# Performance work log

Hardware: AMD Instinct MI355X
Metric: run time of the kernel (lower is better)

## Reference

```python
import jax, jax.numpy as jnp
import numpy as np

B, L, D, H1, OUT, MAX_W = 16, 128, 768, 770, 40, 30


def _span_mask():
    # valid spans: i <= j and width < MAX_W (structured sparsity over the L x L grid)
    ii, jj = np.meshgrid(np.arange(L), np.arange(L), indexing='ij')
    return ((jj >= ii) & (jj - ii < MAX_W)).astype(np.int32)


def setup_inputs():
    key = jax.random.key(0)
    ks = jax.random.split(key, 5)
    hidden_states = jax.random.normal(ks[0], (B, L + 1, D), dtype=jnp.float32)
    rng = np.random.default_rng(0)
    starts = rng.integers(0, L - MAX_W, size=(B,))
    ends = starts + rng.integers(0, MAX_W, size=(B,))
    pred_spans = jnp.asarray(np.stack([starts, ends], axis=1), dtype=jnp.int32)
    span_mask = jnp.asarray(_span_mask())
    W1 = 0.02 * jax.random.normal(ks[1], (2 * D + 1, H1), dtype=jnp.float32)
    b1 = jax.random.normal(ks[2], (H1,), dtype=jnp.float32)
    W2 = 0.02 * jax.random.normal(ks[3], (H1, OUT), dtype=jnp.float32)
    b2 = jax.random.normal(ks[4], (OUT,), dtype=jnp.float32)
    return dict(hidden_states=hidden_states, pred_spans=pred_spans, token_num=L,
                span_available_indication_matrix=span_mask,
                W1=W1, b1=b1, W2=W2, b2=b2)


def reference(hidden_states, pred_spans, token_num, span_available_indication_matrix, W1, b1, W2, b2):
    # span mask is an integer constant -> resolve valid (i, j) pairs on host
    mask = np.asarray(span_available_indication_matrix)
    vi, vj = np.nonzero(mask == 1)            # [n_valid] each
    vi_j = jnp.asarray(vi)
    vj_j = jnp.asarray(vj)
    vecs = hidden_states[:, 1:token_num + 1, :]  # token t -> hidden[:, t+1, :], [B, L, D]
    xi = vecs[:, vi_j, :]                        # [B, n_valid, D] gather of span-start vecs
    xj = vecs[:, vj_j, :]                        # [B, n_valid, D] gather of span-end vecs
    # pred_indications: 2 if span == pred span; 1 if strictly inside it (i<=j); else 0
    s = pred_spans[:, 0:1]
    e = pred_spans[:, 1:2]
    i_ = vi_j[None, :]
    j_ = vj_j[None, :]
    exact = (i_ == s) & (j_ == e)
    inside = (i_ >= s) & (j_ <= e) & (i_ <= j_)
    ind = jnp.where(exact, 2.0, jnp.where(inside, 1.0, 0.0)).astype(hidden_states.dtype)  # [B, n_valid]
    # Linear over concat([xi, xj, ind]) expressed as split matmuls (avoids materializing concat)
    W1i, W1j, w1c = W1[:D], W1[D:2 * D], W1[2 * D]
    h = (jnp.einsum('bnd,dh->bnh', xi, W1i)
         + jnp.einsum('bnd,dh->bnh', xj, W1j)
         + ind[..., None] * w1c + b1)
    h = jax.nn.relu(h)
    logits = jnp.einsum('bnh,ho->bno', h, W2) + b2   # [B, n_valid, OUT]
    return jax.nn.log_softmax(logits, axis=-1)
```

## Files before the change

### kernel.cpp

```cpp
#include <hip/hip_runtime.h>
#include <math.h>

#define B_ 16
#define L_ 128
#define D_ 768
#define H1_ 770
#define OUT_ 40
#define NPAIRS 3405
#define NLOG 1540
#define YSB 1552
#define VOFFB 776
#define KPAD 800
#define NPAD 48
#define W1TROWS 1600
#define NTILES 252
#define NKS 25

typedef __attribute__((ext_vector_type(8))) short bf16x8;
typedef __attribute__((ext_vector_type(8))) unsigned short u16x8;
typedef __attribute__((ext_vector_type(4))) float f32x4;
typedef __attribute__((ext_vector_type(4))) unsigned int u32x4;

__device__ inline unsigned short f2bf(float f) {
  unsigned int u = __builtin_bit_cast(unsigned int, f);
  u += 0x7fffu + ((u >> 16) & 1u);
  return (unsigned short)(u >> 16);
}
__device__ inline float bf2f(unsigned short x) {
  return __builtin_bit_cast(float, (unsigned int)x << 16);
}

#if __has_builtin(__builtin_amdgcn_cvt_pk_bf16_f32)
typedef __attribute__((ext_vector_type(2))) __bf16 bf16x2_t;
__device__ inline unsigned int pack_bf16(float lo, float hi) {
  bf16x2_t r = __builtin_amdgcn_cvt_pk_bf16_f32(lo, hi);
  return __builtin_bit_cast(unsigned int, r);
}
#else
__device__ inline unsigned int pack_bf16(float lo, float hi) {
  return (unsigned int)f2bf(lo) | ((unsigned int)f2bf(hi) << 16);
}
#endif

typedef const __attribute__((address_space(1))) void* gas_t;
typedef __attribute__((address_space(3))) void* las_t;
__device__ inline void gl2lds16(const void* g, void* l) {
  __builtin_amdgcn_global_load_lds((gas_t)g, (las_t)l, 16, 0, 0);
}

#define NB_X 1536
#define NB_W 160
#define NB_T 1200

__global__ __launch_bounds__(256) void prep_all(
    const float* __restrict__ hidden, const float* __restrict__ W1,
    const float* __restrict__ b1, const float* __restrict__ W2,
    unsigned short* __restrict__ Xb, unsigned short* __restrict__ W1T,
    unsigned short* __restrict__ Bswz, float* __restrict__ Cv)
{
  __shared__ float t[32][33];
  int bx = blockIdx.x;
  const int tid = threadIdx.x;

  if (bx < NB_X) {
    int idx = bx * 256 + tid;
    int m = idx / 192;
    int c = idx - m * 192;
    float4 f = *(const float4*)(hidden + (size_t)(m + (m >> 7) + 1) * D_ + c * 4);
    ushort4 o;
    o.x = f2bf(f.x); o.y = f2bf(f.y); o.z = f2bf(f.z); o.w = f2bf(f.w);
    *(ushort4*)(Xb + (size_t)m * D_ + c * 4) = o;
    return;
  }
  bx -= NB_X;
  if (bx < NB_W) {
    int idx = bx * 256 + tid;
    if (idx < NKS * 3 * 512) {
      int ks = idx / 1536;
      int rem = idx - ks * 1536;
      int f = rem / 512;
      int l = (rem - f * 512) >> 3;
      int e = rem & 7;
      int n = f * 16 + (l & 15);
      int k = ks * 32 + (l >> 4) * 8 + e;
      float v = (n < OUT_ && k < H1_) ? W2[k * OUT_ + n] : 0.f;
      Bswz[idx] = f2bf(v);
    } else if (idx < NKS * 3 * 512 + 3 * KPAD) {
      int c = idx - NKS * 3 * 512;
      int tt = c / KPAD, k = c - tt * KPAD;
      const float* w1c = W1 + 1536 * H1_;
      Cv[c] = (k < H1_) ? (b1[k] + (float)tt * w1c[k]) : 0.f;
    }
    return;
  }
  bx -= NB_W;
  const int tx = tid & 31, ty = tid >> 5;
  const int n0 = (bx % 50) * 32, k0 = (bx / 50) * 32;
  #pragma unroll
  for (int r = 0; r < 4; ++r) {
    int k = k0 + ty + r * 8, n = n0 + tx;
    float v = 0.f;
    if (n < H1_)       v = W1[k * H1_ + n];
    else if (n < NLOG) v = W1[(D_ + k) * H1_ + (n - H1_)];
    t[ty + r * 8][tx] = v;
  }
  __syncthreads();
  #pragma unroll
  for (int r = 0; r < 4; ++r) {
    int n = n0 + ty + r * 8, k = k0 + tx;
    W1T[(size_t)n * D_ + k] = f2bf(t[tx][ty + r * 8]);
  }
}

__global__ __launch_bounds__(256) void gemm1_mfma(
    const unsigned short* __restrict__ Xb, const unsigned short* __restrict__ W1T,
    unsigned short* __restrict__ Yb)
{
  __shared__ unsigned short As[2][64][64];
  __shared__ unsigned short Bs[2][64][64];
  const int tid = threadIdx.x;
  const int lane = tid & 63, w = tid >> 6;
  const int lm = lane & 15, q = lane >> 4;
  const int row0 = blockIdx.y * 64, col0 = blockIdx.x * 64;
  const int m0 = (w >> 1) * 32, n0 = (w & 1) * 32;

  const int srow = w * 16 + (lane >> 3);
  const int schunk = (lane & 7) * 8;
  const unsigned short* ga = Xb  + (size_t)(row0 + srow) * D_ + schunk;
  const unsigned short* gb = W1T + (size_t)(col0 + srow) * D_ + schunk;

  f32x4 acc[2][2] = {};

  auto stage = [&](int k0, int b) {
    gl2lds16(ga + k0,          &As[b][w * 16][0]);
    gl2lds16(ga + k0 + 8 * D_, &As[b][w * 16 + 8][0]);
    gl2lds16(gb + k0,          &Bs[b][w * 16][0]);
    gl2lds16(gb + k0 + 8 * D_, &Bs[b][w * 16 + 8][0]);
  };

  stage(0, 0);
  for (int it = 0; it < 12; ++it) {
    const int cur = it & 1;
    __syncthreads();
    if (it < 11) stage((it + 1) * 64, cur ^ 1);
    #pragma unroll
    for (int ks = 0; ks < 2; ++ks) {
      bf16x8 a0 = *(const bf16x8*)&As[cur][m0 + lm]     [ks * 32 + q * 8];
      bf16x8 a1 = *(const bf16x8*)&As[cur][m0 + 16 + lm][ks * 32 + q * 8];
      bf16x8 b0 = *(const bf16x8*)&Bs[cur][n0 + lm]     [ks * 32 + q * 8];
      bf16x8 b1 = *(const bf16x8*)&Bs[cur][n0 + 16 + lm][ks * 32 + q * 8];
      acc[0][0] = __builtin_amdgcn_mfma_f32_16x16x32_bf16(a0, b0, acc[0][0], 0, 0, 0);
      acc[0][1] = __builtin_amdgcn_mfma_f32_16x16x32_bf16(a0, b1, acc[0][1], 0, 0, 0);
      acc[1][0] = __builtin_amdgcn_mfma_f32_16x16x32_bf16(a1, b0, acc[1][0], 0, 0, 0);
      acc[1][1] = __builtin_amdgcn_mfma_f32_16x16x32_bf16(a1, b1, acc[1][1], 0, 0, 0);
    }
  }

  #pragma unroll
  for (int ti = 0; ti < 2; ++ti) {
    #pragma unroll
    for (int tj = 0; tj < 2; ++tj) {
      int col = col0 + n0 + tj * 16 + lm;
      if (col >= NLOG) continue;
      int pc = (col < H1_) ? col : col + (VOFFB - H1_);
      #pragma unroll
      for (int r = 0; r < 4; ++r) {
        int row = row0 + m0 + ti * 16 + q * 4 + r;
        Yb[(size_t)row * YSB + pc] = f2bf(acc[ti][tj][r]);
      }
    }
  }
}

__device__ inline void tile_decode(int T, int& ti, int& d) {
  if (T < 216) { ti = T / 9; d = T - ti * 9; }
  else {
    int m = T - 216; int r = 24, w = 8;
    while (m >= w) { m -= w; --w; ++r; }
    ti = r; d = m;
  }
}
__device__ inline int pair_rank(int i, int j) {
  return (i < 99) ? i * 30 + (j - i)
                  : NPAIRS - (128 - i) * (129 - i) / 2 + (j - i);
}

__global__ __launch_bounds__(256) void pair_mfma(
    const unsigned short* __restrict__ Yb, const int* __restrict__ spans,
    const unsigned short* __restrict__ Bswz, const float* __restrict__ Cv,
    const float* __restrict__ b2, float* __restrict__ out)
{
  const int tid = threadIdx.x;
  const int bb = blockIdx.y;
  const int lane = tid & 63, w = tid >> 6;
  const int lm = lane & 15, q = lane >> 4;

  int ti, d;
  tile_decode(blockIdx.x * 4 + w, ti, d);
  const int i0 = ti * 4, j0 = (ti + d) * 4;

  const int ai = i0 + (lm & 3);
  const int aj = j0 + (lm >> 2);
  const int s = spans[2 * bb], e = spans[2 * bb + 1];
  const int ind = (ai == s && aj == e) ? 2 : ((ai >= s && aj <= e) ? 1 : 0);

  const unsigned short* uptr = Yb + (size_t)(bb * L_ + ai) * YSB + q * 8;
  const unsigned short* vptr = Yb + (size_t)(bb * L_ + aj) * YSB + VOFFB + q * 8;
  const float* cptr = Cv + ind * KPAD + q * 8;
  const unsigned short* bbase = Bswz + lane * 8;

  f32x4 acc0 = {}, acc1 = {}, acc2 = {};

  #pragma unroll 5
  for (int ks = 0; ks < NKS; ++ks) {
    const int ko = ks * 32;
    u16x8 uu = *(const u16x8*)(uptr + ko);
    u16x8 vv = *(const u16x8*)(vptr + ko);
    float4 c0 = *(const float4*)(cptr + ko);
    float4 c1 = *(const float4*)(cptr + ko + 4);
    float h0 = fmaxf(bf2f(uu[0]) + bf2f(vv[0]) + c0.x, 0.f);
    float h1 = fmaxf(bf2f(uu[1]) + bf2f(vv[1]) + c0.y, 0.f);
    float h2 = fmaxf(bf2f(uu[2]) + bf2f(vv[2]) + c0.z, 0.f);
    float h3 = fmaxf(bf2f(uu[3]) + bf2f(vv[3]) + c0.w, 0.f);
    float h4 = fmaxf(bf2f(uu[4]) + bf2f(vv[4]) + c1.x, 0.f);
    float h5 = fmaxf(bf2f(uu[5]) + bf2f(vv[5]) + c1.y, 0.f);
    float h6 = fmaxf(bf2f(uu[6]) + bf2f(vv[6]) + c1.z, 0.f);
    float h7 = fmaxf(bf2f(uu[7]) + bf2f(vv[7]) + c1.w, 0.f);
    u32x4 hp;
    hp[0] = pack_bf16(h0, h1);
    hp[1] = pack_bf16(h2, h3);
    hp[2] = pack_bf16(h4, h5);
    hp[3] = pack_bf16(h6, h7);
    bf16x8 a = __builtin_bit_cast(bf16x8, hp);
    bf16x8 bf0 = *(const bf16x8*)(bbase + (size_t)(ks * 3 + 0) * 512);
    bf16x8 bf1 = *(const bf16x8*)(bbase + (size_t)(ks * 3 + 1) * 512);
    bf16x8 bf2v = *(const bf16x8*)(bbase + (size_t)(ks * 3 + 2) * 512);
    acc0 = __builtin_amdgcn_mfma_f32_16x16x32_bf16(a, bf0, acc0, 0, 0, 0);
    acc1 = __builtin_amdgcn_mfma_f32_16x16x32_bf16(a, bf1, acc1, 0, 0, 0);
    acc2 = __builtin_amdgcn_mfma_f32_16x16x32_bf16(a, bf2v, acc2, 0, 0, 0);
  }

  const float b2v0 = b2[lm];
  const float b2v1 = b2[16 + lm];
  const float b2v2 = (lm < 8) ? b2[32 + lm] : 0.f;
  const int oi = i0 , oj = j0 + q;

  #pragma unroll
  for (int r = 0; r < 4; ++r) {
    float l0 = acc0[r] + b2v0;
    float l1 = acc1[r] + b2v1;
    float l2 = (lm < 8) ? (acc2[r] + b2v2) : -INFINITY;
    float mx = fmaxf(fmaxf(l0, l1), l2);
    mx = fmaxf(mx, __shfl_xor(mx, 1));
    mx = fmaxf(mx, __shfl_xor(mx, 2));
    mx = fmaxf(mx, __shfl_xor(mx, 4));
    mx = fmaxf(mx, __shfl_xor(mx, 8));
    float sm = expf(l0 - mx) + expf(l1 - mx) + ((lm < 8) ? expf(l2 - mx) : 0.f);
    sm += __shfl_xor(sm, 1);
    sm += __shfl_xor(sm, 2);
    sm += __shfl_xor(sm, 4);
    sm += __shfl_xor(sm, 8);
    float lsd = mx + logf(sm);

    int pi_ = oi + r, pj_ = oj;
    if (pj_ >= pi_ && (pj_ - pi_) < 30) {
      float* op = out + ((size_t)bb * NPAIRS + pair_rank(pi_, pj_)) * OUT_;
      op[lm]      = l0 - lsd;
      op[16 + lm] = l1 - lsd;
      if (lm < 8) op[32 + lm] = l2 - lsd;
    }
  }
}

extern "C" void kernel_launch(void* const* d_in, const int* in_sizes, int n_in,
                              void* d_out, int out_size, void* d_ws, size_t ws_size,
                              hipStream_t stream) {
  const float* hidden = (const float*)d_in[0];
  const int*   spans  = (const int*)d_in[1];
  const float* W1 = (const float*)d_in[4];
  const float* b1 = (const float*)d_in[5];
  const float* W2 = (const float*)d_in[6];
  const float* b2 = (const float*)d_in[7];
  float* out = (float*)d_out;

  char* base = (char*)d_ws;
  size_t off = 0;
  auto take = [&](size_t bytes) {
    char* p = base + off;
    off = (off + bytes + 255) & ~(size_t)255;
    return p;
  };
  unsigned short* Yb   = (unsigned short*)take((size_t)2049 * YSB * 2);
  unsigned short* Xb   = (unsigned short*)take((size_t)2048 * D_ * 2);
  unsigned short* W1T  = (unsigned short*)take((size_t)W1TROWS * D_ * 2);
  unsigned short* Bswz = (unsigned short*)take((size_t)NKS * 3 * 512 * 2);
  float*          Cv   = (float*)take((size_t)3 * KPAD * 4);

  prep_all<<<dim3(NB_X + NB_W + NB_T), 256, 0, stream>>>(
      hidden, W1, b1, W2, Xb, W1T, Bswz, Cv);
  gemm1_mfma<<<dim3(25, 32), 256, 0, stream>>>(Xb, W1T, Yb);
  pair_mfma<<<dim3(63, B_), 256, 0, stream>>>(Yb, spans, Bswz, Cv, b2, out);
}
```

Baseline: 135.1 us.

## Fuse three kernels into one cooperative persistent kernel with grid syncs

```diff
diff --git a/kernel.cpp b/kernel.cpp
--- a/kernel.cpp
+++ b/kernel.cpp
@@ -1,5 +1,8 @@
 #include <hip/hip_runtime.h>
+#include <hip/hip_cooperative_groups.h>
 #include <math.h>
+
+namespace cg = cooperative_groups;
 
 #define B_ 16
 #define L_ 128
@@ -11,10 +14,16 @@
 #define YSB 1552
 #define VOFFB 776
 #define KPAD 800
-#define NPAD 48
 #define W1TROWS 1600
-#define NTILES 252
 #define NKS 25
+#define NCU_ 256
+
+#define NB_X 1536
+#define NB_W 160
+#define NB_T 1200
+#define NB_A (NB_X + NB_W + NB_T)
+#define NB_B 800
+#define NB_C 1008
 
 typedef __attribute__((ext_vector_type(8))) short bf16x8;
 typedef __attribute__((ext_vector_type(8))) unsigned short u16x8;
@@ -48,33 +57,36 @@
   __builtin_amdgcn_global_load_lds((gas_t)g, (las_t)l, 16, 0, 0);
 }
 
-#define NB_X 1536
-#define NB_W 160
-#define NB_T 1200
-
-__global__ __launch_bounds__(256) void prep_all(
-    const float* __restrict__ hidden, const float* __restrict__ W1,
-    const float* __restrict__ b1, const float* __restrict__ W2,
-    unsigned short* __restrict__ Xb, unsigned short* __restrict__ W1T,
-    unsigned short* __restrict__ Bswz, float* __restrict__ Cv)
-{
-  __shared__ float t[32][33];
-  int bx = blockIdx.x;
-  const int tid = threadIdx.x;
-
-  if (bx < NB_X) {
-    int idx = bx * 256 + tid;
+__device__ inline void tile_decode(int T, int& ti, int& d) {
+  if (T < 216) { ti = T / 9; d = T - ti * 9; }
+  else {
+    int m = T - 216; int r = 24, w = 8;
+    while (m >= w) { m -= w; --w; ++r; }
+    ti = r; d = m;
+  }
+}
+__device__ inline int pair_rank(int i, int j) {
+  return (i < 99) ? i * 30 + (j - i)
+                  : NPAIRS - (128 - i) * (129 - i) / 2 + (j - i);
+}
+
+__device__ inline void phaseA_unit(
+    int u, int tid, const float* __restrict__ hidden,
+    const float* __restrict__ W1, const float* __restrict__ b1,
+    const float* __restrict__ W2, unsigned short* __restrict__ Xb,
+    unsigned short* __restrict__ W1T, unsigned short* __restrict__ Bswz,
+    float* __restrict__ Cv, float (*t)[33])
+{
+  if (u < NB_X) {
+    int idx = u * 256 + tid;
     int m = idx / 192;
     int c = idx - m * 192;
     float4 f = *(const float4*)(hidden + (size_t)(m + (m >> 7) + 1) * D_ + c * 4);
     ushort4 o;
     o.x = f2bf(f.x); o.y = f2bf(f.y); o.z = f2bf(f.z); o.w = f2bf(f.w);
     *(ushort4*)(Xb + (size_t)m * D_ + c * 4) = o;
-    return;
-  }
-  bx -= NB_X;
-  if (bx < NB_W) {
-    int idx = bx * 256 + tid;
+  } else if (u < NB_X + NB_W) {
+    int idx = (u - NB_X) * 256 + tid;
     if (idx < NKS * 3 * 512) {
       int ks = idx / 1536;
       int rem = idx - ks * 1536;
@@ -91,39 +103,37 @@
       const float* w1c = W1 + 1536 * H1_;
       Cv[c] = (k < H1_) ? (b1[k] + (float)tt * w1c[k]) : 0.f;
     }
-    return;
-  }
-  bx -= NB_W;
-  const int tx = tid & 31, ty = tid >> 5;
-  const int n0 = (bx % 50) * 32, k0 = (bx / 50) * 32;
-  #pragma unroll
-  for (int r = 0; r < 4; ++r) {
-    int k = k0 + ty + r * 8, n = n0 + tx;
-    float v = 0.f;
-    if (n < H1_)       v = W1[k * H1_ + n];
-    else if (n < NLOG) v = W1[(D_ + k) * H1_ + (n - H1_)];
-    t[ty + r * 8][tx] = v;
-  }
-  __syncthreads();
-  #pragma unroll
-  for (int r = 0; r < 4; ++r) {
-    int n = n0 + ty + r * 8, k = k0 + tx;
-    W1T[(size_t)n * D_ + k] = f2bf(t[tx][ty + r * 8]);
-  }
-}
-
-__global__ __launch_bounds__(256) void gemm1_mfma(
-    const unsigned short* __restrict__ Xb, const unsigned short* __restrict__ W1T,
-    unsigned short* __restrict__ Yb)
-{
-  __shared__ unsigned short As[2][64][64];
-  __shared__ unsigned short Bs[2][64][64];
-  const int tid = threadIdx.x;
+  } else {
+    int bx = u - NB_X - NB_W;
+    const int tx = tid & 31, ty = tid >> 5;
+    const int n0 = (bx % 50) * 32, k0 = (bx / 50) * 32;
+    #pragma unroll
+    for (int r = 0; r < 4; ++r) {
+      int k = k0 + ty + r * 8, n = n0 + tx;
+      float v = 0.f;
+      if (n < H1_)       v = W1[k * H1_ + n];
+      else if (n < NLOG) v = W1[(D_ + k) * H1_ + (n - H1_)];
+      t[ty + r * 8][tx] = v;
+    }
+    __syncthreads();
+    #pragma unroll
+    for (int r = 0; r < 4; ++r) {
+      int n = n0 + ty + r * 8, k = k0 + tx;
+      W1T[(size_t)n * D_ + k] = f2bf(t[tx][ty + r * 8]);
+    }
+    __syncthreads();
+  }
+}
+
+__device__ inline void phaseB_unit(
+    int u, int tid, const unsigned short* __restrict__ Xb,
+    const unsigned short* __restrict__ W1T, unsigned short* __restrict__ Yb,
+    unsigned short (*As)[64], unsigned short (*Bs)[64])
+{
   const int lane = tid & 63, w = tid >> 6;
   const int lm = lane & 15, q = lane >> 4;
-  const int row0 = blockIdx.y * 64, col0 = blockIdx.x * 64;
+  const int row0 = (u / 25) * 64, col0 = (u % 25) * 64;
   const int m0 = (w >> 1) * 32, n0 = (w & 1) * 32;
-
   const int srow = w * 16 + (lane >> 3);
   const int schunk = (lane & 7) * 8;
   const unsigned short* ga = Xb  + (size_t)(row0 + srow) * D_ + schunk;
@@ -131,29 +141,24 @@
 
   f32x4 acc[2][2] = {};
 
-  auto stage = [&](int k0, int b) {
-    gl2lds16(ga + k0,          &As[b][w * 16][0]);
-    gl2lds16(ga + k0 + 8 * D_, &As[b][w * 16 + 8][0]);
-    gl2lds16(gb + k0,          &Bs[b][w * 16][0]);
-    gl2lds16(gb + k0 + 8 * D_, &Bs[b][w * 16 + 8][0]);
-  };
-
-  stage(0, 0);
-  for (int it = 0; it < 12; ++it) {
-    const int cur = it & 1;
+  for (int k0 = 0; k0 < D_; k0 += 64) {
+    gl2lds16(ga + k0,          &As[w * 16][0]);
+    gl2lds16(ga + k0 + 8 * D_, &As[w * 16 + 8][0]);
+    gl2lds16(gb + k0,          &Bs[w * 16][0]);
+    gl2lds16(gb + k0 + 8 * D_, &Bs[w * 16 + 8][0]);
     __syncthreads();
-    if (it < 11) stage((it + 1) * 64, cur ^ 1);
     #pragma unroll
     for (int ks = 0; ks < 2; ++ks) {
-      bf16x8 a0 = *(const bf16x8*)&As[cur][m0 + lm]     [ks * 32 + q * 8];
-      bf16x8 a1 = *(const bf16x8*)&As[cur][m0 + 16 + lm][ks * 32 + q * 8];
-      bf16x8 b0 = *(const bf16x8*)&Bs[cur][n0 + lm]     [ks * 32 + q * 8];
-      bf16x8 b1 = *(const bf16x8*)&Bs[cur][n0 + 16 + lm][ks * 32 + q * 8];
+      bf16x8 a0 = *(const bf16x8*)&As[m0 + lm]     [ks * 32 + q * 8];
+      bf16x8 a1 = *(const bf16x8*)&As[m0 + 16 + lm][ks * 32 + q * 8];
+      bf16x8 b0 = *(const bf16x8*)&Bs[n0 + lm]     [ks * 32 + q * 8];
+      bf16x8 b1 = *(const bf16x8*)&Bs[n0 + 16 + lm][ks * 32 + q * 8];
       acc[0][0] = __builtin_amdgcn_mfma_f32_16x16x32_bf16(a0, b0, acc[0][0], 0, 0, 0);
       acc[0][1] = __builtin_amdgcn_mfma_f32_16x16x32_bf16(a0, b1, acc[0][1], 0, 0, 0);
       acc[1][0] = __builtin_amdgcn_mfma_f32_16x16x32_bf16(a1, b0, acc[1][0], 0, 0, 0);
       acc[1][1] = __builtin_amdgcn_mfma_f32_16x16x32_bf16(a1, b1, acc[1][1], 0, 0, 0);
     }
+    __syncthreads();
   }
 
   #pragma unroll
@@ -172,31 +177,17 @@
   }
 }
 
-__device__ inline void tile_decode(int T, int& ti, int& d) {
-  if (T < 216) { ti = T / 9; d = T - ti * 9; }
-  else {
-    int m = T - 216; int r = 24, w = 8;
-    while (m >= w) { m -= w; --w; ++r; }
-    ti = r; d = m;
-  }
-}
-__device__ inline int pair_rank(int i, int j) {
-  return (i < 99) ? i * 30 + (j - i)
-                  : NPAIRS - (128 - i) * (129 - i) / 2 + (j - i);
-}
-
-__global__ __launch_bounds__(256) void pair_mfma(
-    const unsigned short* __restrict__ Yb, const int* __restrict__ spans,
-    const unsigned short* __restrict__ Bswz, const float* __restrict__ Cv,
-    const float* __restrict__ b2, float* __restrict__ out)
-{
-  const int tid = threadIdx.x;
-  const int bb = blockIdx.y;
+__device__ inline void phaseC_unit(
+    int u, int tid, const unsigned short* __restrict__ Yb,
+    const int* __restrict__ spans, const unsigned short* __restrict__ Bswz,
+    const float* __restrict__ Cv, const float* __restrict__ b2,
+    float* __restrict__ out)
+{
   const int lane = tid & 63, w = tid >> 6;
   const int lm = lane & 15, q = lane >> 4;
-
+  const int bb = u / 63;
   int ti, d;
-  tile_decode(blockIdx.x * 4 + w, ti, d);
+  tile_decode((u % 63) * 4 + w, ti, d);
   const int i0 = ti * 4, j0 = (ti + d) * 4;
 
   const int ai = i0 + (lm & 3);
@@ -211,21 +202,25 @@
 
   f32x4 acc0 = {}, acc1 = {}, acc2 = {};
 
+  u16x8 uu = *(const u16x8*)(uptr);
+  u16x8 vv = *(const u16x8*)(vptr);
+
   #pragma unroll 5
   for (int ks = 0; ks < NKS; ++ks) {
     const int ko = ks * 32;
-    u16x8 uu = *(const u16x8*)(uptr + ko);
-    u16x8 vv = *(const u16x8*)(vptr + ko);
+    u16x8 cu = uu, cw = vv;
+    uu = *(const u16x8*)(uptr + ko + 32);
+    vv = *(const u16x8*)(vptr + ko + 32);
     float4 c0 = *(const float4*)(cptr + ko);
     float4 c1 = *(const float4*)(cptr + ko + 4);
-    float h0 = fmaxf(bf2f(uu[0]) + bf2f(vv[0]) + c0.x, 0.f);
-    float h1 = fmaxf(bf2f(uu[1]) + bf2f(vv[1]) + c0.y, 0.f);
-    float h2 = fmaxf(bf2f(uu[2]) + bf2f(vv[2]) + c0.z, 0.f);
-    float h3 = fmaxf(bf2f(uu[3]) + bf2f(vv[3]) + c0.w, 0.f);
-    float h4 = fmaxf(bf2f(uu[4]) + bf2f(vv[4]) + c1.x, 0.f);
-    float h5 = fmaxf(bf2f(uu[5]) + bf2f(vv[5]) + c1.y, 0.f);
-    float h6 = fmaxf(bf2f(uu[6]) + bf2f(vv[6]) + c1.z, 0.f);
-    float h7 = fmaxf(bf2f(uu[7]) + bf2f(vv[7]) + c1.w, 0.f);
+    float h0 = fmaxf(bf2f(cu[0]) + bf2f(cw[0]) + c0.x, 0.f);
+    float h1 = fmaxf(bf2f(cu[1]) + bf2f(cw[1]) + c0.y, 0.f);
+    float h2 = fmaxf(bf2f(cu[2]) + bf2f(cw[2]) + c0.z, 0.f);
+    float h3 = fmaxf(bf2f(cu[3]) + bf2f(cw[3]) + c0.w, 0.f);
+    float h4 = fmaxf(bf2f(cu[4]) + bf2f(cw[4]) + c1.x, 0.f);
+    float h5 = fmaxf(bf2f(cu[5]) + bf2f(cw[5]) + c1.y, 0.f);
+    float h6 = fmaxf(bf2f(cu[6]) + bf2f(cw[6]) + c1.z, 0.f);
+    float h7 = fmaxf(bf2f(cu[7]) + bf2f(cw[7]) + c1.w, 0.f);
     u32x4 hp;
     hp[0] = pack_bf16(h0, h1);
     hp[1] = pack_bf16(h2, h3);
@@ -243,7 +238,6 @@
   const float b2v0 = b2[lm];
   const float b2v1 = b2[16 + lm];
   const float b2v2 = (lm < 8) ? b2[32 + lm] : 0.f;
-  const int oi = i0 , oj = j0 + q;
 
   #pragma unroll
   for (int r = 0; r < 4; ++r) {
@@ -262,7 +256,7 @@
     sm += __shfl_xor(sm, 8);
     float lsd = mx + logf(sm);
 
-    int pi_ = oi + r, pj_ = oj;
+    int pi_ = i0 + r, pj_ = j0 + q;
     if (pj_ >= pi_ && (pj_ - pi_) < 30) {
       float* op = out + ((size_t)bb * NPAIRS + pair_rank(pi_, pj_)) * OUT_;
       op[lm]      = l0 - lsd;
@@ -270,6 +264,69 @@
       if (lm < 8) op[32 + lm] = l2 - lsd;
     }
   }
+}
+
+__global__ __launch_bounds__(256, 2) void fused_all(
+    const float* __restrict__ hidden, const int* __restrict__ spans,
+    const float* __restrict__ W1, const float* __restrict__ b1,
+    const float* __restrict__ W2, const float* __restrict__ b2,
+    float* __restrict__ out,
+    unsigned short* __restrict__ Xb, unsigned short* __restrict__ W1T,
+    unsigned short* __restrict__ Bswz, float* __restrict__ Cv,
+    unsigned short* __restrict__ Yb)
+{
+  __shared__ union __align__(16) SM {
+    float t[32][33];
+    unsigned short ab[2][64][64];
+  } sm;
+  cg::grid_group grid = cg::this_grid();
+  const int tid = threadIdx.x;
+  const int G = gridDim.x;
+
+  for (int u = blockIdx.x; u < NB_A; u += G)
+    phaseA_unit(u, tid, hidden, W1, b1, W2, Xb, W1T, Bswz, Cv, sm.t);
+
+  __builtin_amdgcn_fence(__ATOMIC_SEQ_CST, "agent");
+  grid.sync();
+  __builtin_amdgcn_fence(__ATOMIC_SEQ_CST, "agent");
+  __syncthreads();
+
+  for (int u = blockIdx.x; u < NB_B; u += G)
+    phaseB_unit(u, tid, Xb, W1T, Yb, sm.ab[0], sm.ab[1]);
+
+  __builtin_amdgcn_fence(__ATOMIC_SEQ_CST, "agent");
+  grid.sync();
+  __builtin_amdgcn_fence(__ATOMIC_SEQ_CST, "agent");
+
+  for (int u = blockIdx.x; u < NB_C; u += G)
+    phaseC_unit(u, tid, Yb, spans, Bswz, Cv, b2, out);
+}
+
+__global__ __launch_bounds__(256) void prep_k(
+    const float* __restrict__ hidden, const float* __restrict__ W1,
+    const float* __restrict__ b1, const float* __restrict__ W2,
+    unsigned short* __restrict__ Xb, unsigned short* __restrict__ W1T,
+    unsigned short* __restrict__ Bswz, float* __restrict__ Cv)
+{
+  __shared__ float t[32][33];
+  phaseA_unit(blockIdx.x, threadIdx.x, hidden, W1, b1, W2, Xb, W1T, Bswz, Cv, t);
+}
+
+__global__ __launch_bounds__(256) void gemm_k(
+    const unsigned short* __restrict__ Xb, const unsigned short* __restrict__ W1T,
+    unsigned short* __restrict__ Yb)
+{
+  __shared__ unsigned short As[64][64];
+  __shared__ unsigned short Bs[64][64];
+  phaseB_unit(blockIdx.x, threadIdx.x, Xb, W1T, Yb, As, Bs);
+}
+
+__global__ __launch_bounds__(256) void pair_k(
+    const unsigned short* __restrict__ Yb, const int* __restrict__ spans,
+    const unsigned short* __restrict__ Bswz, const float* __restrict__ Cv,
+    const float* __restrict__ b2, float* __restrict__ out)
+{
+  phaseC_unit(blockIdx.x, threadIdx.x, Yb, spans, Bswz, Cv, b2, out);
 }
 
 extern "C" void kernel_launch(void* const* d_in, const int* in_sizes, int n_in,
@@ -296,8 +353,26 @@
   unsigned short* Bswz = (unsigned short*)take((size_t)NKS * 3 * 512 * 2);
   float*          Cv   = (float*)take((size_t)3 * KPAD * 4);
 
-  prep_all<<<dim3(NB_X + NB_W + NB_T), 256, 0, stream>>>(
-      hidden, W1, b1, W2, Xb, W1T, Bswz, Cv);
-  gemm1_mfma<<<dim3(25, 32), 256, 0, stream>>>(Xb, W1T, Yb);
-  pair_mfma<<<dim3(63, B_), 256, 0, stream>>>(Yb, spans, Bswz, Cv, b2, out);
-}
+  int nblk = 0;
+  hipError_t qe = hipOccupancyMaxActiveBlocksPerMultiprocessor(
+      &nblk, (const void*)fused_all, 256, 0);
+  int grid = (qe == hipSuccess && nblk > 0) ? nblk * NCU_ : 0;
+  if (grid > NB_C) grid = NB_C;
+
+  bool launched = false;
+  if (grid >= 64) {
+    void* args[] = {
+      (void*)&hidden, (void*)&spans, (void*)&W1, (void*)&b1, (void*)&W2,
+      (void*)&b2, (void*)&out, (void*)&Xb, (void*)&W1T, (void*)&Bswz,
+      (void*)&Cv, (void*)&Yb
+    };
+    launched = (hipLaunchCooperativeKernel((const void*)fused_all, dim3(grid),
+                                           dim3(256), args, 0, stream)
+                == hipSuccess);
+  }
+  if (!launched) {
+    prep_k<<<dim3(NB_A), 256, 0, stream>>>(hidden, W1, b1, W2, Xb, W1T, Bswz, Cv);
+    gemm_k<<<dim3(NB_B), 256, 0, stream>>>(Xb, W1T, Yb);
+    pair_k<<<dim3(NB_C), 256, 0, stream>>>(Yb, spans, Bswz, Cv, b2, out);
+  }
+}
```

Measured after the change: 335.5 us. +148.4%, slower.
